# Optimization experiments

Hardware: AMD Instinct MI355X
Metric: run time of the kernel (lower is better)

The kernel has to match this reference:

```python
import jax, jax.numpy as jnp
import numpy as np

N_NODES = 50000
N_EDGES = 800000
NUM_GRAPHS = 128
KS = 5           # kernel_size per pseudo dim
K = KS * KS      # 25 spline weight matrices per layer


def spline_coeff(pseudo):
    """Open linear (degree-1) B-spline basis for 2-D pseudo coords in [0,1].
    Returns dense per-edge coefficients over the K=25 kernel slots: [E, K]."""
    pos = pseudo * (KS - 1)                      # [E,2]
    lo = jnp.clip(jnp.floor(pos).astype(jnp.int32), 0, KS - 2)
    frac = pos - lo.astype(pseudo.dtype)         # [E,2]
    i0, i1 = lo, lo + 1
    w0, w1 = 1.0 - frac, frac
    # 2^dim = 4 corner combinations, flat index = d0 + KS*d1
    idx = jnp.stack([i0[:, 0] + KS * i0[:, 1],
                     i0[:, 0] + KS * i1[:, 1],
                     i1[:, 0] + KS * i0[:, 1],
                     i1[:, 0] + KS * i1[:, 1]], axis=1)            # [E,4]
    w = jnp.stack([w0[:, 0] * w0[:, 1], w0[:, 0] * w1[:, 1],
                   w1[:, 0] * w0[:, 1], w1[:, 0] * w1[:, 1]], axis=1)  # [E,4]
    E = pseudo.shape[0]
    coeff = jnp.zeros((E, K), pseudo.dtype).at[jnp.arange(E)[:, None], idx].add(w)
    return coeff


def spline_conv(x, coeff, src, dst, W, root, bias):
    """SplineConv: gather src feats, spline-weighted transform, scatter-mean to dst,
    plus root weight and bias. x:[N,in], coeff:[E,K], W:[K,in,out]."""
    n = x.shape[0]
    x_src = x[src]                                # [E,in] gather
    m = coeff[:, 0:1] * (x_src @ W[0])            # [E,out]
    for k in range(1, K):                         # fixed small loop over K kernels
        m = m + coeff[:, k:k + 1] * (x_src @ W[k])
    agg = jax.ops.segment_sum(m, dst, num_segments=n)
    cnt = jax.ops.segment_sum(jnp.ones((src.shape[0],), x.dtype), dst, num_segments=n)
    agg = agg / jnp.maximum(cnt, 1.0)[:, None]    # mean aggregation (PyG default)
    return agg + x @ root + bias


def setup_inputs() -> dict:
    key = jax.random.key(0)
    ks = jax.random.split(key, 16)
    s = 0.1  # small init scale for numerical stability
    return {
        "x": jax.random.normal(ks[0], (N_NODES, 1), jnp.float32),
        "position": jax.random.uniform(ks[1], (N_NODES, 2), jnp.float32),
        "pseudo": jax.random.uniform(ks[2], (N_EDGES, 2), jnp.float32),
        "edge_index": jax.random.randint(ks[3], (2, N_EDGES), 0, N_NODES, jnp.int32),
        "batch": jnp.sort(jax.random.randint(ks[4], (N_NODES,), 0, NUM_GRAPHS, jnp.int32)),
        "W1": s * jax.random.normal(ks[5], (K, 1, 32), jnp.float32),
        "root1": s * jax.random.normal(ks[6], (1, 32), jnp.float32),
        "b1": jnp.zeros((32,), jnp.float32),
        "W2": s * jax.random.normal(ks[7], (K, 32, 64), jnp.float32),
        "root2": s * jax.random.normal(ks[8], (32, 64), jnp.float32),
        "b2": jnp.zeros((64,), jnp.float32),
        "W3": s * jax.random.normal(ks[9], (K, 64, 64), jnp.float32),
        "root3": s * jax.random.normal(ks[10], (64, 64), jnp.float32),
        "b3": jnp.zeros((64,), jnp.float32),
        "fc_w": s * jax.random.normal(ks[11], (64, 10), jnp.float32),
        "fc_b": jnp.zeros((10,), jnp.float32),
    }


def reference(x, position, pseudo, edge_index, batch,
              W1, root1, b1, W2, root2, b2, W3, root3, b3, fc_w, fc_b):
    # `position` is accepted but unused, matching the original forward.
    src, dst = edge_index[0], edge_index[1]
    coeff = spline_coeff(pseudo)
    h = jax.nn.elu(spline_conv(x, coeff, src, dst, W1, root1, b1))
    h = jax.nn.elu(spline_conv(h, coeff, src, dst, W2, root2, b2))
    h = jax.nn.elu(spline_conv(h, coeff, src, dst, W3, root3, b3))
    # scatter_mean pooling over batch indices -> [NUM_GRAPHS, 64]
    pooled = jax.ops.segment_sum(h, batch, num_segments=NUM_GRAPHS)
    gcnt = jax.ops.segment_sum(jnp.ones((h.shape[0],), h.dtype), batch,
                               num_segments=NUM_GRAPHS)
    pooled = pooled / jnp.maximum(gcnt, 1.0)[:, None]
    # dropout is identity in eval mode
    logits = pooled @ fc_w + fc_b
    return jax.nn.log_softmax(logits, axis=1)
```

## Files before the change

kernel.cpp:

```cpp
#include <hip/hip_runtime.h>

#define NN 50000
#define NE 800000
#define NG 128
#define NB_SCAN 196

typedef unsigned int uint;
typedef unsigned short ushort;
typedef __attribute__((ext_vector_type(8))) short short8;
typedef __attribute__((ext_vector_type(4))) float f32x4;
typedef __attribute__((ext_vector_type(16))) float f32x16;

__device__ __forceinline__ float bf2f(ushort u){ union{uint i; float f;} v; v.i=(uint)u<<16; return v.f; }
__device__ __forceinline__ ushort f2bf(float f){ union{float f; uint i;} v; v.f=f; return (ushort)((v.i + 0x7FFFu + ((v.i>>16)&1u))>>16); }
__device__ __forceinline__ int iswz(int i){ return i ^ ((i>>4)&3); }

__global__ void zero_k(int* hist, float* pooled, int* gcnt){
    int i = blockIdx.x*blockDim.x + threadIdx.x;
    if (i < NN) hist[i] = 0;
    if (i < NG*64) pooled[i] = 0.f;
    if (i < NG) gcnt[i] = 0;
}

__global__ void hist_k(const int* __restrict__ ei, int* __restrict__ hist){
    int e = blockIdx.x*blockDim.x + threadIdx.x;
    if (e < NE) atomicAdd(&hist[ei[NE + e]], 1);
}

__global__ __launch_bounds__(256) void scan1(const int* __restrict__ hist, int* __restrict__ bsum){
    __shared__ int sm[256];
    int t = threadIdx.x, i = blockIdx.x*256 + t;
    sm[t] = (i < NN) ? hist[i] : 0;
    __syncthreads();
    for (int o = 128; o > 0; o >>= 1){ if (t < o) sm[t] += sm[t+o]; __syncthreads(); }
    if (t == 0) bsum[blockIdx.x] = sm[0];
}
__global__ __launch_bounds__(256) void scan2(const int* __restrict__ bsum, int* __restrict__ bpre){
    __shared__ int sm[256];
    int t = threadIdx.x;
    int v = (t < NB_SCAN) ? bsum[t] : 0;
    sm[t] = v; __syncthreads();
    int acc = v;
    for (int o = 1; o < 256; o <<= 1){
        int u = (t >= o) ? sm[t-o] : 0; __syncthreads();
        acc += u; sm[t] = acc; __syncthreads();
    }
    if (t < NB_SCAN) bpre[t] = acc - v;
}
__global__ __launch_bounds__(256) void scan3(const int* __restrict__ hist, const int* __restrict__ bpre,
                                             int* __restrict__ offs, int* __restrict__ cursor,
                                             float* __restrict__ invc){
    __shared__ int sm[256];
    int t = threadIdx.x, b = blockIdx.x, i = b*256 + t;
    int v = (i < NN) ? hist[i] : 0;
    sm[t] = v; __syncthreads();
    int acc = v;
    for (int o = 1; o < 256; o <<= 1){
        int u = (t >= o) ? sm[t-o] : 0; __syncthreads();
        acc += u; sm[t] = acc; __syncthreads();
    }
    int excl = acc - v + bpre[b];
    if (i < NN){ offs[i] = excl; cursor[i] = excl; invc[i] = 1.0f/(float)max(v,1); }
    if (i == NN-1) offs[NN] = NE;
}

__global__ void scatter_k(const int* __restrict__ ei, const float* __restrict__ pseudo,
                          int* __restrict__ cursor, uint4* __restrict__ payA, uint* __restrict__ payB){
    int e = blockIdx.x*blockDim.x + threadIdx.x;
    if (e >= NE) return;
    float2 ps = *(const float2*)(pseudo + 2*(size_t)e);
    float px = ps.x * 4.0f, py = ps.y * 4.0f;
    int lx = min(max((int)floorf(px), 0), 3);
    int ly = min(max((int)floorf(py), 0), 3);
    float fx = px - (float)lx, fy = py - (float)ly;
    float gx = 1.f - fx, gy = 1.f - fy;
    float w00 = gx*gy, w10 = fx*gy, w01 = gx*fy, w11 = fx*fy;
    ushort h00 = f2bf(w00), h10 = f2bf(w10), h01 = f2bf(w01), h11 = f2bf(w11);
    ushort L00 = f2bf(w00 - bf2f(h00)), L10 = f2bf(w10 - bf2f(h10));
    ushort L01 = f2bf(w01 - bf2f(h01)), L11 = f2bf(w11 - bf2f(h11));
    uint meta = (uint)ei[e] | ((uint)lx<<16) | ((uint)ly<<18);
    int pos = atomicAdd(&cursor[ei[NE + e]], 1);
    payA[pos] = make_uint4(meta, (uint)h00 | ((uint)h10<<16),
                                 (uint)h01 | ((uint)h11<<16),
                                 (uint)L00 | ((uint)L10<<16));
    payB[pos] = (uint)L01 | ((uint)L11<<16);
}

template<int IN>
__global__ void wprep_k(const float* __restrict__ W, const float* __restrict__ root, ushort* __restrict__ Bp){
    const int total = 26*IN*64;
    int tid = blockIdx.x*blockDim.x + threadIdx.x;
    if (tid >= total) return;
    int j    = tid & 7;
    int lane = (tid >> 3) & 63;
    int ctkt = tid >> 9;
    int ct   = ctkt & 3;
    int kt   = ctkt >> 2;
    int kk   = kt*32 + (lane>>4)*8 + j;
    int col  = ct*16 + (lane & 15);
    float v;
    if (kk < 25*IN){ int k = kk / IN; int i = kk % IN; v = W[((size_t)k*IN + i)*64 + col]; }
    else           { v = root[(size_t)(kk - 25*IN)*64 + col]; }
    Bp[tid] = f2bf(v);
}

__global__ __launch_bounds__(256) void reduce1_k(const float* __restrict__ x, const uint4* __restrict__ payA,
                                                 const uint* __restrict__ payB,
                                                 const int* __restrict__ offs, const float* __restrict__ invc,
                                                 const float* __restrict__ W1, const float* __restrict__ root1,
                                                 const float* __restrict__ b1, ushort* __restrict__ h1bf){
    __shared__ float w1s[25*32];
    for (int i = threadIdx.x; i < 25*32; i += 256) w1s[i] = W1[i];
    __syncthreads();
    int wid  = threadIdx.x >> 6;
    int lane = threadIdx.x & 63;
    int o    = lane & 31;
    int half = lane >> 5;
    int d    = blockIdx.x*4 + wid;
    int s = offs[d], e = offs[d+1];
    float acc = 0.f;
    for (int p = s; p < e; ++p){
        uint4 q0 = payA[p];
        uint lo23 = payB[p];
        uint meta = q0.x;
        int lx = (meta>>16)&3, ly = (meta>>18)&3;
        float wa, wb;
        if (half == 0){ wa = bf2f((ushort)q0.y) + bf2f((ushort)q0.w);
                        wb = bf2f((ushort)q0.z) + bf2f((ushort)lo23); }
        else          { wa = bf2f((ushort)(q0.y>>16)) + bf2f((ushort)(q0.w>>16));
                        wb = bf2f((ushort)(q0.z>>16)) + bf2f((ushort)(lo23>>16)); }
        float xs = x[meta & 0xFFFF];
        int ka = ly*5 + lx + half;
        acc += (wa*w1s[ka*32 + o] + wb*w1s[(ka+5)*32 + o]) * xs;
    }
    acc += __shfl_xor(acc, 32);
    if (half == 0){
        float val = acc*invc[d] + x[d]*root1[o] + b1[o];
        val = val > 0.f ? val : expm1f(val);
        h1bf[(size_t)d*32 + o] = f2bf(val);
    }
}

template<int MODE>
__global__ __launch_bounds__(512) void fused32(
        const ushort* __restrict__ hin, const uint4* __restrict__ payA, const uint* __restrict__ payB,
        const int* __restrict__ offs, const float* __restrict__ invc,
        const ushort* __restrict__ Bp, const float* __restrict__ bias,
        const int* __restrict__ batch, ushort* __restrict__ hout,
        float* __restrict__ pooled, int* __restrict__ gcnt)
{
    constexpr int KT = 26, KH = 13;
    __shared__ __align__(16) ushort Sb[KT*512];
    __shared__ __align__(16) uint4 eA[8][16];
    __shared__ uint eB[8][16];
    __shared__ float red[1024];
    __shared__ float outS[1024];

    const int tid = threadIdx.x, lane = tid & 63, w = tid >> 6;
    const int ln31 = lane & 31, kg2 = lane >> 5;
    const int d0 = blockIdx.x * 16;
    const int i0 = ln31 % 5, j0 = ln31 / 5;
    const bool rv = (ln31 < 25);

    for (int nn = 0; nn < 2; ++nn){
        const int node = w*2 + nn;
        const int d = d0 + node;
        int s = offs[d];
        int h = offs[d+1] - s;
        int steps = (h + 15) >> 4;

        f32x16 accH;
        #pragma unroll
        for (int q = 0; q < 16; ++q) accH[q] = 0.f;

        uint4 vA = make_uint4(0u,0u,0u,0u); uint vB = 0u;
        {
            int rem = (h < 16) ? h : 16;
            if (lane < rem) vA = payA[(size_t)s + lane];
            int j2 = lane - 16;
            if (j2 >= 0 && j2 < rem) vB = payB[(size_t)s + j2];
        }
        for (int ks = 0; ks < steps; ++ks){
            if (lane < 16) eA[w][lane] = vA;
            else if (lane < 32) eB[w][lane-16] = vB;
            if (ks+1 < steps){
                int rem = h - (ks+1)*16; if (rem > 16) rem = 16;
                uint4 nA = make_uint4(0u,0u,0u,0u); uint nB = 0u;
                if (lane < rem) nA = payA[(size_t)(s + (ks+1)*16) + lane];
                int j2 = lane - 16;
                if (j2 >= 0 && j2 < rem) nB = payB[(size_t)(s + (ks+1)*16) + j2];
                vA = nA; vB = nB;
            }
            short8 ah, al;
            uint srcs[8];
            #pragma unroll
            for (int j = 0; j < 8; ++j){
                int es = kg2*8 + j;
                uint4 q0  = eA[w][es];
                uint lo23 = eB[w][es];
                uint meta = q0.x;
                int lx = (meta>>16)&3, ly = (meta>>18)&3;
                int dx = i0 - lx, dy = j0 - ly;
                bool ok = rv && ((uint)dx < 2u) && ((uint)dy < 2u);
                uint hiw = (dy == 1) ? q0.z : q0.y;
                uint low = (dy == 1) ? lo23 : q0.w;
                int sh = (dx & 1) << 4;
                ah[j] = ok ? (short)((hiw >> sh) & 0xFFFFu) : (short)0;
                al[j] = ok ? (short)((low >> sh) & 0xFFFFu) : (short)0;
                srcs[j] = meta & 0xFFFFu;
            }
            short8 bfv;
            #pragma unroll
            for (int j = 0; j < 8; ++j)
                bfv[j] = (short)hin[(size_t)srcs[j]*32 + ln31];
            accH = __builtin_amdgcn_mfma_f32_32x32x16_bf16(ah, bfv, accH, 0, 0, 0);
            accH = __builtin_amdgcn_mfma_f32_32x32x16_bf16(al, bfv, accH, 0, 0, 0);
        }

        {
            float ic = invc[d];
            int jd  = ln31 & 7;
            int l3  = ln31 >> 3;
            #pragma unroll
            for (int reg = 0; reg < 16; ++reg){
                int r = (reg & 3) + 8*(reg >> 2) + 4*kg2;
                if (r < 25)
                    Sb[r*512 + iswz(l3*16 + node)*8 + jd] = f2bf(accH[reg]*ic);
            }
            if (lane < 32)
                Sb[25*512 + iswz(((lane>>3)&3)*16 + node)*8 + (lane&7)] = hin[(size_t)d*32 + lane];
        }
    }
    __syncthreads();

    {
        int ct = w & 3, kh = w >> 2;
        int c15 = lane & 15, kg = lane >> 4;
        int ig = iswz(lane);
        f32x4 a4 = {0.f,0.f,0.f,0.f};
        const ushort* bb = Bp + ct*512 + (size_t)lane*8;
        #pragma unroll
        for (int k = 0; k < KH; ++k){
            int kt = kh*KH + k;
            short8 a = *(const short8*)(Sb + kt*512 + ig*8);
            short8 b = *(const short8*)(bb + (size_t)kt*2048);
            a4 = __builtin_amdgcn_mfma_f32_16x16x32_bf16(a, b, a4, 0, 0, 0);
        }
        if (kh == 1){
            float* rr = red + (ct*64 + lane)*4;
            rr[0]=a4[0]; rr[1]=a4[1]; rr[2]=a4[2]; rr[3]=a4[3];
        }
        __syncthreads();
        if (kh == 0){
            const float* rr = red + (ct*64 + lane)*4;
            int col = ct*16 + c15;
            float bs = bias[col];
            #pragma unroll
            for (int jq = 0; jq < 4; ++jq){
                int r16 = kg*4 + jq;
                float v = a4[jq] + rr[jq] + bs;
                v = v > 0.f ? v : expm1f(v);
                if (MODE == 0) ((ushort*)outS)[r16*64 + col] = f2bf(v);
                else           outS[r16*64 + col] = v;
            }
        }
    }
    __syncthreads();

    if (MODE == 0){
        uint* dst = (uint*)(hout + (size_t)d0*64);
        dst[tid] = ((const uint*)outS)[tid];
    } else {
        if (w == 0){
            int c = lane;
            float run = 0.f; int gprev = batch[d0];
            for (int r = 0; r < 16; ++r){
                int g = batch[d0 + r];
                if (g != gprev){ atomicAdd(&pooled[gprev*64 + c], run); run = 0.f; gprev = g; }
                run += outS[r*64 + c];
            }
            atomicAdd(&pooled[gprev*64 + c], run);
        } else if (w == 1 && lane == 0){
            int cnt = 0; int gprev = batch[d0];
            for (int r = 0; r < 16; ++r){
                int g = batch[d0 + r];
                if (g != gprev){ atomicAdd(&gcnt[gprev], cnt); cnt = 0; gprev = g; }
                cnt++;
            }
            atomicAdd(&gcnt[gprev], cnt);
        }
    }
}

template<int MODE>
__global__ __launch_bounds__(512) void fused64(
        const ushort* __restrict__ hin, const uint4* __restrict__ payA, const uint* __restrict__ payB,
        const int* __restrict__ offs, const float* __restrict__ invc,
        const ushort* __restrict__ Bp, const float* __restrict__ bias,
        const int* __restrict__ batch, ushort* __restrict__ hout,
        float* __restrict__ pooled, int* __restrict__ gcnt)
{
    __shared__ __align__(16) ushort Sb[26*512];
    __shared__ __align__(16) uint4 eA[8][16];
    __shared__ uint eB[8][16];
    __shared__ float red[1024];
    __shared__ float outS[512];

    const int tid = threadIdx.x, lane = tid & 63, w = tid >> 6;
    const int ln31 = lane & 31, kg2 = lane >> 5;
    const int d0 = blockIdx.x * 8;
    const int d  = d0 + w;
    const int i0 = ln31 % 5, j0 = ln31 / 5;
    const bool rv = (ln31 < 25);

    int s = offs[d];
    int h = offs[d+1] - s;
    int steps = (h + 15) >> 4;

    f32x16 acc0, acc1;
    #pragma unroll
    for (int q = 0; q < 16; ++q){ acc0[q] = 0.f; acc1[q] = 0.f; }

    {
        uint4 vA = make_uint4(0u,0u,0u,0u); uint vB = 0u;
        {
            int rem = (h < 16) ? h : 16;
            if (lane < rem) vA = payA[(size_t)s + lane];
            int j2 = lane - 16;
            if (j2 >= 0 && j2 < rem) vB = payB[(size_t)s + j2];
        }
        for (int ks = 0; ks < steps; ++ks){
            if (lane < 16) eA[w][lane] = vA;
            else if (lane < 32) eB[w][lane-16] = vB;
            if (ks+1 < steps){
                int rem = h - (ks+1)*16; if (rem > 16) rem = 16;
                uint4 nA = make_uint4(0u,0u,0u,0u); uint nB = 0u;
                if (lane < rem) nA = payA[(size_t)(s + (ks+1)*16) + lane];
                int j2 = lane - 16;
                if (j2 >= 0 && j2 < rem) nB = payB[(size_t)(s + (ks+1)*16) + j2];
                vA = nA; vB = nB;
            }
            short8 ah, al;
            uint hx[8];
            #pragma unroll
            for (int j = 0; j < 8; ++j){
                int es = kg2*8 + j;
                uint4 q0  = eA[w][es];
                uint lo23 = eB[w][es];
                uint meta = q0.x;
                int lx = (meta>>16)&3, ly = (meta>>18)&3;
                int dx = i0 - lx, dy = j0 - ly;
                bool ok = rv && ((uint)dx < 2u) && ((uint)dy < 2u);
                uint hiw = (dy == 1) ? q0.z : q0.y;
                uint low = (dy == 1) ? lo23 : q0.w;
                int sh = (dx & 1) << 4;
                ah[j] = ok ? (short)((hiw >> sh) & 0xFFFFu) : (short)0;
                al[j] = ok ? (short)((low >> sh) & 0xFFFFu) : (short)0;
                hx[j] = *(const uint*)(hin + (size_t)(meta & 0xFFFFu)*64 + 2*ln31);
            }
            short8 b0, b1;
            #pragma unroll
            for (int j = 0; j < 8; ++j){
                b0[j] = (short)(ushort)hx[j];
                b1[j] = (short)(ushort)(hx[j] >> 16);
            }
            acc0 = __builtin_amdgcn_mfma_f32_32x32x16_bf16(ah, b0, acc0, 0, 0, 0);
            acc0 = __builtin_amdgcn_mfma_f32_32x32x16_bf16(al, b0, acc0, 0, 0, 0);
            acc1 = __builtin_amdgcn_mfma_f32_32x32x16_bf16(ah, b1, acc1, 0, 0, 0);
            acc1 = __builtin_amdgcn_mfma_f32_32x32x16_bf16(al, b1, acc1, 0, 0, 0);
        }
    }

    float ic = invc[d];
    int ct = w & 3, g = w >> 2;
    int c15 = lane & 15;
    int ig = iswz(lane);
    f32x4 a4 = {0.f,0.f,0.f,0.f};
    const ushort* bb = Bp + ct*512 + (size_t)lane*8;

    #pragma unroll
    for (int P = 0; P < 2; ++P){
        #pragma unroll
        for (int reg = 0; reg < 16; ++reg){
            int r = (reg & 3) + 8*(reg >> 2) + 4*kg2;
            int rl = r - P*13;
            if (rl >= 0 && rl < 13 && r < 25){
                int off0 = 2*ln31;
                int ktl0 = rl*2 + (off0>>5);
                int kgp  = (off0>>3)&3;
                int jd0  = off0&7;
                int gsl  = iswz(kgp*16 + w)*8;
                Sb[ktl0*512 + gsl + jd0]     = f2bf(acc0[reg]*ic);
                Sb[ktl0*512 + gsl + jd0 + 1] = f2bf(acc1[reg]*ic);
            }
        }
        if (P == 1){
            int f = lane;
            Sb[(24 + (f>>5))*512 + iswz(((f>>3)&3)*16 + w)*8 + (f&7)] = hin[(size_t)d*64 + f];
        }
        __syncthreads();
        #pragma unroll
        for (int k = 0; k < 13; ++k){
            int ktl = g*13 + k;
            int ktg = P*26 + ktl;
            short8 a = *(const short8*)(Sb + ktl*512 + ig*8);
            short8 b = *(const short8*)(bb + (size_t)ktg*2048);
            a4 = __builtin_amdgcn_mfma_f32_16x16x32_bf16(a, b, a4, 0, 0, 0);
        }
        __syncthreads();
    }

    if (g == 1) *(f32x4*)&red[(ct*64 + lane)*4] = a4;
    __syncthreads();
    if (g == 0){
        f32x4 rr = *(const f32x4*)&red[(ct*64 + lane)*4];
        int kg = lane >> 4;
        int col = ct*16 + c15;
        float bs = bias[col];
        #pragma unroll
        for (int jq = 0; jq < 4; ++jq){
            int r8 = kg*4 + jq;
            if (r8 < 8){
                float v = a4[jq] + rr[jq] + bs;
                v = v > 0.f ? v : expm1f(v);
                if (MODE == 0) ((ushort*)outS)[r8*64 + col] = f2bf(v);
                else           outS[r8*64 + col] = v;
            }
        }
    }
    __syncthreads();

    if (MODE == 0){
        if (tid < 256){
            uint* dst = (uint*)(hout + (size_t)d0*64);
            dst[tid] = ((const uint*)outS)[tid];
        }
    } else {
        if (w == 0){
            int c = lane;
            float run = 0.f; int gprev = batch[d0];
            for (int r = 0; r < 8; ++r){
                int gb = batch[d0 + r];
                if (gb != gprev){ atomicAdd(&pooled[gprev*64 + c], run); run = 0.f; gprev = gb; }
                run += outS[r*64 + c];
            }
            atomicAdd(&pooled[gprev*64 + c], run);
        } else if (w == 1 && lane == 0){
            int cnt = 0; int gprev = batch[d0];
            for (int r = 0; r < 8; ++r){
                int gb = batch[d0 + r];
                if (gb != gprev){ atomicAdd(&gcnt[gprev], cnt); cnt = 0; gprev = gb; }
                cnt++;
            }
            atomicAdd(&gcnt[gprev], cnt);
        }
    }
}

__global__ __launch_bounds__(128) void head_k(const float* __restrict__ pooled, const int* __restrict__ gcnt,
                                              const float* __restrict__ fcw, const float* __restrict__ fcb,
                                              float* __restrict__ out){
    int g = threadIdx.x;
    if (g >= NG) return;
    float inv = 1.0f / fmaxf((float)gcnt[g], 1.0f);
    float logits[10];
    #pragma unroll
    for (int c = 0; c < 10; ++c) logits[c] = fcb[c];
    for (int o = 0; o < 64; ++o){
        float m = pooled[g*64 + o] * inv;
        #pragma unroll
        for (int c = 0; c < 10; ++c) logits[c] += m * fcw[o*10 + c];
    }
    float mx = logits[0];
    #pragma unroll
    for (int c = 1; c < 10; ++c) mx = fmaxf(mx, logits[c]);
    float ssum = 0.f;
    #pragma unroll
    for (int c = 0; c < 10; ++c) ssum += expf(logits[c] - mx);
    float lse = logf(ssum) + mx;
    #pragma unroll
    for (int c = 0; c < 10; ++c) out[g*10 + c] = logits[c] - lse;
}

extern "C" void kernel_launch(void* const* d_in, const int* in_sizes, int n_in,
                              void* d_out, int out_size, void* d_ws, size_t ws_size,
                              hipStream_t stream) {
    const float* x      = (const float*)d_in[0];
    const float* pseudo = (const float*)d_in[2];
    const int*   ei     = (const int*)  d_in[3];
    const int*   batch  = (const int*)  d_in[4];
    const float* W1     = (const float*)d_in[5];
    const float* root1  = (const float*)d_in[6];
    const float* b1     = (const float*)d_in[7];
    const float* W2     = (const float*)d_in[8];
    const float* root2  = (const float*)d_in[9];
    const float* b2     = (const float*)d_in[10];
    const float* W3     = (const float*)d_in[11];
    const float* root3  = (const float*)d_in[12];
    const float* b3     = (const float*)d_in[13];
    const float* fcw    = (const float*)d_in[14];
    const float* fcb    = (const float*)d_in[15];
    float* out = (float*)d_out;

    char* ws = (char*)d_ws;
    size_t off = 0;
    auto alloc = [&](size_t bytes)->char*{ char* p = ws + off; off += (bytes + 255) / 256 * 256; return p; };
    uint4*  payA   = (uint4*) alloc((size_t)NE*16);
    uint*   payB   = (uint*)  alloc((size_t)NE*4);
    ushort* h1bf   = (ushort*)alloc((size_t)NN*32*2);
    ushort* h2bf   = (ushort*)alloc((size_t)NN*64*2);
    int*    hist   = (int*)   alloc((size_t)NN*4);
    int*    offs   = (int*)   alloc((size_t)(NN+1)*4);
    int*    cursor = (int*)   alloc((size_t)NN*4);
    float*  invc   = (float*) alloc((size_t)NN*4);
    int*    bsum   = (int*)   alloc((size_t)NB_SCAN*4);
    int*    bpre   = (int*)   alloc((size_t)NB_SCAN*4);
    ushort* Bp2    = (ushort*)alloc((size_t)26*2048*2);
    ushort* Bp3    = (ushort*)alloc((size_t)52*2048*2);
    float*  pooled = (float*) alloc((size_t)NG*64*4);
    int*    gcnt   = (int*)   alloc((size_t)NG*4);
    (void)ws_size; (void)in_sizes; (void)n_in; (void)out_size;

    zero_k   <<<NB_SCAN, 256, 0, stream>>>(hist, pooled, gcnt);
    hist_k   <<<(NE+255)/256, 256, 0, stream>>>(ei, hist);
    scan1    <<<NB_SCAN, 256, 0, stream>>>(hist, bsum);
    scan2    <<<1, 256, 0, stream>>>(bsum, bpre);
    scan3    <<<NB_SCAN, 256, 0, stream>>>(hist, bpre, offs, cursor, invc);
    scatter_k<<<(NE+255)/256, 256, 0, stream>>>(ei, pseudo, cursor, payA, payB);
    wprep_k<32><<<(26*32*64 + 255)/256, 256, 0, stream>>>(W2, root2, Bp2);
    wprep_k<64><<<(26*64*64 + 255)/256, 256, 0, stream>>>(W3, root3, Bp3);
    reduce1_k<<<NN/4, 256, 0, stream>>>(x, payA, payB, offs, invc, W1, root1, b1, h1bf);
    fused32<0><<<NN/16, 512, 0, stream>>>(h1bf, payA, payB, offs, invc, Bp2, b2, batch, h2bf, pooled, gcnt);
    fused64<1><<<NN/8,  512, 0, stream>>>(h2bf, payA, payB, offs, invc, Bp3, b3, batch, h2bf, pooled, gcnt);
    head_k   <<<1, 128, 0, stream>>>(pooled, gcnt, fcw, fcb, out);
}
```

Before: 346.1 us.

## Process 16 nodes per block in layer-3 kernel and unroll layer-1 edge loop

The layer-3 fused kernel now has each wave aggregate two destination nodes, so the whole 52-tile staging buffer is filled once and a single 16-row MFMA pass over the weight matrix runs per block instead of two 8-row passes. This halves the number of weight-matrix reads and barriers per node, at the cost of more shared memory per block and possibly lower occupancy. Separately, the layer-1 reduction loop is unrolled by four so payload and feature loads for several edges are issued together, aiming to hide gather latency.

```diff
diff --git a/kernel.cpp b/kernel.cpp
--- a/kernel.cpp
+++ b/kernel.cpp
@@ -119,20 +119,29 @@
     int d    = blockIdx.x*4 + wid;
     int s = offs[d], e = offs[d+1];
     float acc = 0.f;
-    for (int p = s; p < e; ++p){
-        uint4 q0 = payA[p];
-        uint lo23 = payB[p];
-        uint meta = q0.x;
-        int lx = (meta>>16)&3, ly = (meta>>18)&3;
-        float wa, wb;
-        if (half == 0){ wa = bf2f((ushort)q0.y) + bf2f((ushort)q0.w);
-                        wb = bf2f((ushort)q0.z) + bf2f((ushort)lo23); }
-        else          { wa = bf2f((ushort)(q0.y>>16)) + bf2f((ushort)(q0.w>>16));
-                        wb = bf2f((ushort)(q0.z>>16)) + bf2f((ushort)(lo23>>16)); }
-        float xs = x[meta & 0xFFFF];
-        int ka = ly*5 + lx + half;
-        acc += (wa*w1s[ka*32 + o] + wb*w1s[(ka+5)*32 + o]) * xs;
-    }
+#define E1(QA, LO, XS) { uint meta = (QA).x; \
+    int lx = (meta>>16)&3, ly = (meta>>18)&3; \
+    float wa, wb; \
+    if (half == 0){ wa = bf2f((ushort)(QA).y) + bf2f((ushort)(QA).w); \
+                    wb = bf2f((ushort)(QA).z) + bf2f((ushort)(LO)); } \
+    else          { wa = bf2f((ushort)((QA).y>>16)) + bf2f((ushort)((QA).w>>16)); \
+                    wb = bf2f((ushort)((QA).z>>16)) + bf2f((ushort)((LO)>>16)); } \
+    int ka = ly*5 + lx + half; \
+    acc += (wa*w1s[ka*32 + o] + wb*w1s[(ka+5)*32 + o]) * (XS); }
+    int p = s;
+    for (; p + 4 <= e; p += 4){
+        uint4 a0 = payA[p], a1 = payA[p+1], a2 = payA[p+2], a3 = payA[p+3];
+        uint  l0 = payB[p], l1 = payB[p+1], l2 = payB[p+2], l3 = payB[p+3];
+        float x0 = x[a0.x & 0xFFFF], x1 = x[a1.x & 0xFFFF];
+        float x2 = x[a2.x & 0xFFFF], x3 = x[a3.x & 0xFFFF];
+        E1(a0, l0, x0) E1(a1, l1, x1) E1(a2, l2, x2) E1(a3, l3, x3)
+    }
+    for (; p < e; ++p){
+        uint4 a0 = payA[p]; uint l0 = payB[p];
+        float x0 = x[a0.x & 0xFFFF];
+        E1(a0, l0, x0)
+    }
+#undef E1
     acc += __shfl_xor(acc, 32);
     if (half == 0){
         float val = acc*invc[d] + x[d]*root1[o] + b1[o];
@@ -300,28 +309,30 @@
         const int* __restrict__ batch, ushort* __restrict__ hout,
         float* __restrict__ pooled, int* __restrict__ gcnt)
 {
-    __shared__ __align__(16) ushort Sb[26*512];
+    constexpr int KT = 52, KH = 26;
+    __shared__ __align__(16) ushort Sb[KT*512];
     __shared__ __align__(16) uint4 eA[8][16];
     __shared__ uint eB[8][16];
     __shared__ float red[1024];
-    __shared__ float outS[512];
+    __shared__ float outS[1024];
 
     const int tid = threadIdx.x, lane = tid & 63, w = tid >> 6;
     const int ln31 = lane & 31, kg2 = lane >> 5;
-    const int d0 = blockIdx.x * 8;
-    const int d  = d0 + w;
+    const int d0 = blockIdx.x * 16;
     const int i0 = ln31 % 5, j0 = ln31 / 5;
     const bool rv = (ln31 < 25);
 
-    int s = offs[d];
-    int h = offs[d+1] - s;
-    int steps = (h + 15) >> 4;
-
-    f32x16 acc0, acc1;
-    #pragma unroll
-    for (int q = 0; q < 16; ++q){ acc0[q] = 0.f; acc1[q] = 0.f; }
-
-    {
+    for (int nn = 0; nn < 2; ++nn){
+        const int node = w*2 + nn;
+        const int d = d0 + node;
+        int s = offs[d];
+        int h = offs[d+1] - s;
+        int steps = (h + 15) >> 4;
+
+        f32x16 acc0, acc1;
+        #pragma unroll
+        for (int q = 0; q < 16; ++q){ acc0[q] = 0.f; acc1[q] = 0.f; }
+
         uint4 vA = make_uint4(0u,0u,0u,0u); uint vB = 0u;
         {
             int rem = (h < 16) ? h : 16;
@@ -369,87 +380,81 @@
             acc1 = __builtin_amdgcn_mfma_f32_32x32x16_bf16(ah, b1, acc1, 0, 0, 0);
             acc1 = __builtin_amdgcn_mfma_f32_32x32x16_bf16(al, b1, acc1, 0, 0, 0);
         }
-    }
-
-    float ic = invc[d];
-    int ct = w & 3, g = w >> 2;
-    int c15 = lane & 15;
-    int ig = iswz(lane);
-    f32x4 a4 = {0.f,0.f,0.f,0.f};
-    const ushort* bb = Bp + ct*512 + (size_t)lane*8;
-
-    #pragma unroll
-    for (int P = 0; P < 2; ++P){
+
+        {
+            float ic = invc[d];
+            int off0 = 2*ln31;
+            int fhi  = ln31 >> 4;
+            int kgp  = (off0 >> 3) & 3;
+            int jd0  = off0 & 7;
+            int gsl  = iswz(kgp*16 + node)*8;
+            #pragma unroll
+            for (int reg = 0; reg < 16; ++reg){
+                int r = (reg & 3) + 8*(reg >> 2) + 4*kg2;
+                if (r < 25){
+                    int kt = r*2 + fhi;
+                    uint pk = (uint)f2bf(acc0[reg]*ic) | ((uint)f2bf(acc1[reg]*ic) << 16);
+                    *(uint*)(Sb + kt*512 + gsl + jd0) = pk;
+                }
+            }
+            int f = lane;
+            Sb[(50 + (f>>5))*512 + iswz(((f>>3)&3)*16 + node)*8 + (f&7)] = hin[(size_t)d*64 + f];
+        }
+    }
+    __syncthreads();
+
+    {
+        int ct = w & 3, kh = w >> 2;
+        int c15 = lane & 15, kg = lane >> 4;
+        int ig = iswz(lane);
+        f32x4 a4 = {0.f,0.f,0.f,0.f};
+        const ushort* bb = Bp + ct*512 + (size_t)lane*8;
         #pragma unroll
-        for (int reg = 0; reg < 16; ++reg){
-            int r = (reg & 3) + 8*(reg >> 2) + 4*kg2;
-            int rl = r - P*13;
-            if (rl >= 0 && rl < 13 && r < 25){
-                int off0 = 2*ln31;
-                int ktl0 = rl*2 + (off0>>5);
-                int kgp  = (off0>>3)&3;
-                int jd0  = off0&7;
-                int gsl  = iswz(kgp*16 + w)*8;
-                Sb[ktl0*512 + gsl + jd0]     = f2bf(acc0[reg]*ic);
-                Sb[ktl0*512 + gsl + jd0 + 1] = f2bf(acc1[reg]*ic);
-            }
-        }
-        if (P == 1){
-            int f = lane;
-            Sb[(24 + (f>>5))*512 + iswz(((f>>3)&3)*16 + w)*8 + (f&7)] = hin[(size_t)d*64 + f];
+        for (int k = 0; k < KH; ++k){
+            int kt = kh*KH + k;
+            short8 a = *(const short8*)(Sb + kt*512 + ig*8);
+            short8 b = *(const short8*)(bb + (size_t)kt*2048);
+            a4 = __builtin_amdgcn_mfma_f32_16x16x32_bf16(a, b, a4, 0, 0, 0);
+        }
+        if (kh == 1){
+            float* rr = red + (ct*64 + lane)*4;
+            rr[0]=a4[0]; rr[1]=a4[1]; rr[2]=a4[2]; rr[3]=a4[3];
         }
         __syncthreads();
-        #pragma unroll
-        for (int k = 0; k < 13; ++k){
-            int ktl = g*13 + k;
-            int ktg = P*26 + ktl;
-            short8 a = *(const short8*)(Sb + ktl*512 + ig*8);
-            short8 b = *(const short8*)(bb + (size_t)ktg*2048);
-            a4 = __builtin_amdgcn_mfma_f32_16x16x32_bf16(a, b, a4, 0, 0, 0);
-        }
-        __syncthreads();
-    }
-
-    if (g == 1) *(f32x4*)&red[(ct*64 + lane)*4] = a4;
-    __syncthreads();
-    if (g == 0){
-        f32x4 rr = *(const f32x4*)&red[(ct*64 + lane)*4];
-        int kg = lane >> 4;
-        int col = ct*16 + c15;
-        float bs = bias[col];
-        #pragma unroll
-        for (int jq = 0; jq < 4; ++jq){
-            int r8 = kg*4 + jq;
-            if (r8 < 8){
+        if (kh == 0){
+            const float* rr = red + (ct*64 + lane)*4;
+            int col = ct*16 + c15;
+            float bs = bias[col];
+            #pragma unroll
+            for (int jq = 0; jq < 4; ++jq){
+                int r16 = kg*4 + jq;
                 float v = a4[jq] + rr[jq] + bs;
                 v = v > 0.f ? v : expm1f(v);
-                if (MODE == 0) ((ushort*)outS)[r8*64 + col] = f2bf(v);
-                else           outS[r8*64 + col] = v;
+                if (MODE == 0) ((ushort*)outS)[r16*64 + col] = f2bf(v);
+                else           outS[r16*64 + col] = v;
             }
         }
     }
     __syncthreads();
 
     if (MODE == 0){
-        if (tid < 256){
-            uint* dst = (uint*)(hout + (size_t)d0*64);
-            dst[tid] = ((const uint*)outS)[tid];
-        }
+        uint* dst = (uint*)(hout + (size_t)d0*64);
+        dst[tid] = ((const uint*)outS)[tid];
     } else {
         if (w == 0){
             int c = lane;
             float run = 0.f; int gprev = batch[d0];
-            for (int r = 0; r < 8; ++r){
-                int gb = batch[d0 + r];
-                if (gb != gprev){ atomicAdd(&pooled[gprev*64 + c], run); run = 0.f; gprev = gb; }
+            for (int r = 0; r < 16; ++r){
+                int g = batch[d0 + r];
+                if (g != gprev){ atomicAdd(&pooled[gprev*64 + c], run); run = 0.f; gprev = g; }
                 run += outS[r*64 + c];
             }
             atomicAdd(&pooled[gprev*64 + c], run);
         } else if (w == 1 && lane == 0){
             int cnt = 0; int gprev = batch[d0];
-            for (int r = 0; r < 8; ++r){
-                int gb = batch[d0 + r];
-                if (gb != gprev){ atomicAdd(&gcnt[gprev], cnt); cnt = 0; gprev = gb; }
+            for (int r = 0; r < 16; ++r){
+                int g = batch[d0 + r];
+                if (g != gprev){ atomicAdd(&gcnt[gprev], cnt); cnt = 0; gprev = g; }
                 cnt++;
             }
             atomicAdd(&gcnt[gprev], cnt);
@@ -531,6 +536,6 @@
     wprep_k<64><<<(26*64*64 + 255)/256, 256, 0, stream>>>(W3, root3, Bp3);
     reduce1_k<<<NN/4, 256, 0, stream>>>(x, payA, payB, offs, invc, W1, root1, b1, h1bf);
     fused32<0><<<NN/16, 512, 0, stream>>>(h1bf, payA, payB, offs, invc, Bp2, b2, batch, h2bf, pooled, gcnt);
-    fused64<1><<<NN/8,  512, 0, stream>>>(h2bf, payA, payB, offs, invc, Bp3, b3, batch, h2bf, pooled, gcnt);
+    fused64<1><<<NN/16, 512, 0, stream>>>(h2bf, payA, payB, offs, invc, Bp3, b3, batch, h2bf, pooled, gcnt);
     head_k   <<<1, 128, 0, stream>>>(pooled, gcnt, fcw, fcb, out);
 }
```

Result: faster. 286.5 us (-17.2%).
